# Performance work log

Hardware: AMD Instinct MI355X
Metric: run time of the kernel (lower is better)

## Reference

```python
import jax, jax.numpy as jnp
import numpy as np

# Binarize: forward sign(x) in {-1,+1} (sign(0) -> +1), backward straight-through
# estimator (identity gradient), matching the standard ebnn Binarize autograd fn.
@jax.custom_vjp
def binarize(x):
    return jnp.where(x >= 0, 1.0, -1.0).astype(x.dtype)

def _bin_fwd(x):
    return binarize(x), None

def _bin_bwd(_, g):
    return (g,)  # straight-through

binarize.defvjp(_bin_fwd, _bin_bwd)


def setup_inputs() -> dict:
    key = jax.random.key(0)
    kx, kw = jax.random.split(key)
    N, Cin, H, W = 32, 256, 56, 56
    Cout, K = 256, 3
    x = jax.random.normal(kx, (N, Cin, H, W), dtype=jnp.float32)
    # xavier_normal init for conv weight
    fan_in = Cin * K * K
    fan_out = Cout * K * K
    std = float(np.sqrt(2.0 / (fan_in + fan_out)))
    w = jax.random.normal(kw, (Cout, Cin, K, K), dtype=jnp.float32) * std
    b = jnp.zeros((Cout,), dtype=jnp.float32)
    return {"x": x, "w": w, "b": b}


def reference(x, w, b):
    # binarize input (binarize_input=True) and weights, then standard conv2d
    xb = binarize(x)
    wb = binarize(w)
    out = jax.lax.conv_general_dilated(
        xb, wb,
        window_strides=(1, 1),
        padding=((1, 1), (1, 1)),
        rhs_dilation=(1, 1),
        dimension_numbers=("NCHW", "OIHW", "NCHW"),
        feature_group_count=1,
    )
    return out + b[None, :, None, None]
```

## Files before the change

kernel.cpp:

```cpp
#include <hip/hip_runtime.h>
#include <stdint.h>


#define NBATCH 32
#define CIN    256
#define COUT   256
#define HH     56
#define WW     56
#define HW     (HH*WW)
#define NPIX   (NBATCH*HW)

#define PW    58
#define PROW  (PW*8)
#define PIMG  (PW*PW*8)

#define XP_BYTES  ((size_t)NBATCH * PIMG * 4)
#define WQ_BYTES  ((size_t)9 * 8 * 256 * 32)

typedef int i32x4  __attribute__((ext_vector_type(4)));
typedef int i32x16 __attribute__((ext_vector_type(16)));

__global__ __launch_bounds__(256) void pack_x_kernel(
    const float* __restrict__ x, uint32_t* __restrict__ xp)
{
    int lane = threadIdx.x & 63;
    int wv   = threadIdx.x >> 6;
    int pix  = blockIdx.x * 64 + lane;
    int n  = pix / HW;
    int hw = pix - n * HW;
    int h  = hw / WW;
    int w_ = hw - h * WW;
    const float* xb = x + ((size_t)n * CIN + (size_t)wv * 64) * HW + hw;

    uint32_t w0 = 0, w1 = 0;
    #pragma unroll
    for (int j = 0; j < 32; ++j) {
        w0 |= (xb[(size_t)j * HW]        >= 0.0f ? 1u : 0u) << j;
        w1 |= (xb[(size_t)(j + 32) * HW] >= 0.0f ? 1u : 0u) << j;
    }
    uint32_t* dst = xp + (size_t)n * PIMG + (size_t)(h + 1) * PROW
                       + (size_t)(w_ + 1) * 8 + wv * 2;
    *(uint2*)dst = make_uint2(w0, w1);
}

__global__ __launch_bounds__(256) void pack_w2_kernel(
    const float* __restrict__ w, int8_t* __restrict__ wq)
{
    int co = blockIdx.x, ci = threadIdx.x;
    const float* wb = w + ((size_t)co * CIN + ci) * 9;
    int c8 = ci >> 5, s = ci & 31;
    #pragma unroll
    for (int t = 0; t < 9; ++t) {
        wq[((size_t)(t * 8 + c8) * 256 + co) * 32 + s] =
            (wb[t] >= 0.0f) ? (int8_t)1 : (int8_t)-1;
    }
}

__global__ __launch_bounds__(512, 4) void bconv_kernel(
    const uint32_t* __restrict__ xp, const int8_t* __restrict__ wq,
    const float* __restrict__ bias, float* __restrict__ out)
{
    __shared__ __align__(16) int8_t xt[4][66][256];
    __shared__ float bsh[256];

    int bx = blockIdx.x;
    int n  = bx / 28;
    int hb = bx - n * 28;
    int h  = hb * 2;
    int tid = threadIdx.x, lane = tid & 63, wv = tid >> 6;

    if (tid < 256) bsh[tid] = bias[tid];

    const uint32_t* xpb = xp + (size_t)n * PIMG;
    for (int e = tid; e < 4 * 66 * 64; e += 512) {
        int pr  = e / (66 * 64);
        int rem = e - pr * (66 * 64);
        int col = rem >> 6;
        int d   = rem & 63;
        int prg = h + pr;
        bool val = (prg >= 1) & (prg <= 56) & (col >= 1) & (col <= 56);
        uint32_t wvv = 0;
        if (val) wvv = xpb[(size_t)prg * PROW + col * 8 + (d >> 3)];
        uint32_t nib = (wvv >> ((d & 7) * 4)) & 0xFu;
        uint32_t sp  = (nib * 0x00204081u) & 0x01010101u;
        uint32_t o   = val ? __builtin_amdgcn_perm(0u, 0x000001FFu, sp) : 0u;
        uint32_t ba  = (uint32_t)((((pr * 66 + col) << 8) | (d << 2))
                                  ^ ((col & 15) << 4));
        *(uint32_t*)((char*)&xt[0][0][0] + ba) = o;
    }
    __syncthreads();

    int l31  = lane & 31;
    int hi16 = (lane >> 5) << 4;
    const int8_t* wql = wq + ((size_t)(wv * 32 + l31)) * 32 + hi16;
    const char* xtb = (const char*)&xt[0][0][0];

    for (int cb = 0; cb < 2; ++cb) {
        i32x16 accA = {0}, accB = {0};

        for (int dw = 0; dw < 3; ++dw) {
            int col = l31 + cb * 32 + dw;
            int sw  = (col & 15) << 4;
            const char* xc = xtb + (col << 8);
            const int8_t* wa0 = wql + (size_t)(dw * 8) * 8192;
            #pragma unroll
            for (int c8 = 0; c8 < 8; ++c8) {
                int sx = ((c8 << 5) + hi16) ^ sw;
                i32x4 b0 = *(const i32x4*)(xc + ((0 * 66) << 8) + sx);
                i32x4 b1 = *(const i32x4*)(xc + ((1 * 66) << 8) + sx);
                i32x4 b2 = *(const i32x4*)(xc + ((2 * 66) << 8) + sx);
                i32x4 b3 = *(const i32x4*)(xc + ((3 * 66) << 8) + sx);
                const int8_t* wa = wa0 + (size_t)c8 * 8192;
                i32x4 a0v = *(const i32x4*)(wa);
                i32x4 a1v = *(const i32x4*)(wa + 196608);
                i32x4 a2v = *(const i32x4*)(wa + 393216);
                accA = __builtin_amdgcn_mfma_i32_32x32x32_i8(a0v, b0, accA, 0, 0, 0);
                accB = __builtin_amdgcn_mfma_i32_32x32x32_i8(a0v, b1, accB, 0, 0, 0);
                accA = __builtin_amdgcn_mfma_i32_32x32x32_i8(a1v, b1, accA, 0, 0, 0);
                accB = __builtin_amdgcn_mfma_i32_32x32x32_i8(a1v, b2, accB, 0, 0, 0);
                accA = __builtin_amdgcn_mfma_i32_32x32x32_i8(a2v, b2, accA, 0, 0, 0);
                accB = __builtin_amdgcn_mfma_i32_32x32x32_i8(a2v, b3, accB, 0, 0, 0);
            }
        }

        int pix = cb * 32 + l31;
        if (pix < WW) {
            float* op = out + (size_t)n * COUT * HW + (size_t)h * WW + pix;
            #pragma unroll
            for (int r = 0; r < 16; ++r) {
                int row = (r & 3) + 8 * (r >> 2) + ((lane >> 5) << 2);
                int co  = (wv << 5) + row;
                float bb = bsh[co];
                op[(size_t)co * HW]      = (float)accA[r] + bb;
                op[(size_t)co * HW + WW] = (float)accB[r] + bb;
            }
        }
    }
}

extern "C" void kernel_launch(void* const* d_in, const int* in_sizes, int n_in,
                              void* d_out, int out_size, void* d_ws, size_t ws_size,
                              hipStream_t stream) {
    const float* x = (const float*)d_in[0];
    const float* w = (const float*)d_in[1];
    const float* b = (const float*)d_in[2];
    float* out = (float*)d_out;

    uint32_t* xp = (uint32_t*)d_ws;
    int8_t*   wq = (int8_t*)((char*)d_ws + XP_BYTES);

    pack_x_kernel<<<NPIX / 64, 256, 0, stream>>>(x, xp);
    pack_w2_kernel<<<COUT, 256, 0, stream>>>(w, wq);

    bconv_kernel<<<NBATCH * (HH / 2), 512, 0, stream>>>(xp, wq, b, out);
}
```

Baseline: 97.17 us.

## Relayout packed weights per wave and software-pipeline operand loads across MFMA groups

Weights are repacked so that each 32-output-channel group holds its three dh taps for each (dw, c8) step contiguously, 1 KB apart. The inner loop is flattened into 24 fully unrolled steps, and the global weight and LDS activation loads for the next step are issued before the current step's six MFMAs. The goal is to hide load latency behind MFMA work and improve locality of the weight fetches. The cost is more live registers for the double-buffered operands, which could affect occupancy under launch_bounds(512,4).

```diff
diff --git a/kernel.cpp b/kernel.cpp
--- a/kernel.cpp
+++ b/kernel.cpp
@@ -15,7 +15,7 @@
 #define PIMG  (PW*PW*8)
 
 #define XP_BYTES  ((size_t)NBATCH * PIMG * 4)
-#define WQ_BYTES  ((size_t)9 * 8 * 256 * 32)
+#define WQ_BYTES  ((size_t)8 * 72 * 1024)
 
 typedef int i32x4  __attribute__((ext_vector_type(4)));
 typedef int i32x16 __attribute__((ext_vector_type(16)));
@@ -43,21 +43,41 @@
     *(uint2*)dst = make_uint2(w0, w1);
 }
 
-__global__ __launch_bounds__(256) void pack_w2_kernel(
-    const float* __restrict__ w, int8_t* __restrict__ wq)
+__global__ __launch_bounds__(256) void pack_w3_kernel(
+    const float* __restrict__ w, int8_t* __restrict__ wq3)
 {
     int co = blockIdx.x, ci = threadIdx.x;
     const float* wb = w + ((size_t)co * CIN + ci) * 9;
-    int c8 = ci >> 5, s = ci & 31;
+    int cog = co >> 5, l = co & 31, c8 = ci >> 5, s = ci & 31;
+    int8_t* base = wq3 + (size_t)cog * 73728 + (size_t)l * 32 + s;
     #pragma unroll
-    for (int t = 0; t < 9; ++t) {
-        wq[((size_t)(t * 8 + c8) * 256 + co) * 32 + s] =
-            (wb[t] >= 0.0f) ? (int8_t)1 : (int8_t)-1;
+    for (int dh = 0; dh < 3; ++dh) {
+        #pragma unroll
+        for (int dw = 0; dw < 3; ++dw) {
+            int t = dh * 3 + dw;
+            base[(size_t)((dw * 8 + c8) * 3 + dh) * 1024] =
+                (wb[t] >= 0.0f) ? (int8_t)1 : (int8_t)-1;
+        }
     }
 }
 
+#define LOADG(gi, A0, A1, A2, B0, B1, B2, B3) { \
+    const int dw_ = (gi) >> 3, c8_ = (gi) & 7; \
+    const int col_ = l31 + cb * 32 + dw_; \
+    const int sw_ = (col_ & 15) << 4; \
+    const char* xc_ = xtb + (col_ << 8); \
+    const int sx_ = ((c8_ << 5) + hi16) ^ sw_; \
+    B0 = *(const i32x4*)(xc_ + ((0 * 66) << 8) + sx_); \
+    B1 = *(const i32x4*)(xc_ + ((1 * 66) << 8) + sx_); \
+    B2 = *(const i32x4*)(xc_ + ((2 * 66) << 8) + sx_); \
+    B3 = *(const i32x4*)(xc_ + ((3 * 66) << 8) + sx_); \
+    const char* wa_ = wqc + (size_t)((dw_ * 8 + c8_) * 3) * 1024; \
+    A0 = *(const i32x4*)(wa_); \
+    A1 = *(const i32x4*)(wa_ + 1024); \
+    A2 = *(const i32x4*)(wa_ + 2048); }
+
 __global__ __launch_bounds__(512, 4) void bconv_kernel(
-    const uint32_t* __restrict__ xp, const int8_t* __restrict__ wq,
+    const uint32_t* __restrict__ xp, const int8_t* __restrict__ wq3,
     const float* __restrict__ bias, float* __restrict__ out)
 {
     __shared__ __align__(16) int8_t xt[4][66][256];
@@ -92,34 +112,28 @@
 
     int l31  = lane & 31;
     int hi16 = (lane >> 5) << 4;
-    const int8_t* wql = wq + ((size_t)(wv * 32 + l31)) * 32 + hi16;
+    const char* wqc = (const char*)wq3 + (size_t)wv * 73728
+                    + (size_t)l31 * 32 + hi16;
     const char* xtb = (const char*)&xt[0][0][0];
 
     for (int cb = 0; cb < 2; ++cb) {
         i32x16 accA = {0}, accB = {0};
+        i32x4 a0, a1, a2, b0, b1, b2, b3;
+        i32x4 na0, na1, na2, nb0, nb1, nb2, nb3;
 
-        for (int dw = 0; dw < 3; ++dw) {
-            int col = l31 + cb * 32 + dw;
-            int sw  = (col & 15) << 4;
-            const char* xc = xtb + (col << 8);
-            const int8_t* wa0 = wql + (size_t)(dw * 8) * 8192;
-            #pragma unroll
-            for (int c8 = 0; c8 < 8; ++c8) {
-                int sx = ((c8 << 5) + hi16) ^ sw;
-                i32x4 b0 = *(const i32x4*)(xc + ((0 * 66) << 8) + sx);
-                i32x4 b1 = *(const i32x4*)(xc + ((1 * 66) << 8) + sx);
-                i32x4 b2 = *(const i32x4*)(xc + ((2 * 66) << 8) + sx);
-                i32x4 b3 = *(const i32x4*)(xc + ((3 * 66) << 8) + sx);
-                const int8_t* wa = wa0 + (size_t)c8 * 8192;
-                i32x4 a0v = *(const i32x4*)(wa);
-                i32x4 a1v = *(const i32x4*)(wa + 196608);
-                i32x4 a2v = *(const i32x4*)(wa + 393216);
-                accA = __builtin_amdgcn_mfma_i32_32x32x32_i8(a0v, b0, accA, 0, 0, 0);
-                accB = __builtin_amdgcn_mfma_i32_32x32x32_i8(a0v, b1, accB, 0, 0, 0);
-                accA = __builtin_amdgcn_mfma_i32_32x32x32_i8(a1v, b1, accA, 0, 0, 0);
-                accB = __builtin_amdgcn_mfma_i32_32x32x32_i8(a1v, b2, accB, 0, 0, 0);
-                accA = __builtin_amdgcn_mfma_i32_32x32x32_i8(a2v, b2, accA, 0, 0, 0);
-                accB = __builtin_amdgcn_mfma_i32_32x32x32_i8(a2v, b3, accB, 0, 0, 0);
+        LOADG(0, a0, a1, a2, b0, b1, b2, b3)
+        #pragma unroll
+        for (int gi = 0; gi < 24; ++gi) {
+            if (gi < 23) { LOADG(gi + 1, na0, na1, na2, nb0, nb1, nb2, nb3) }
+            accA = __builtin_amdgcn_mfma_i32_32x32x32_i8(a0, b0, accA, 0, 0, 0);
+            accB = __builtin_amdgcn_mfma_i32_32x32x32_i8(a0, b1, accB, 0, 0, 0);
+            accA = __builtin_amdgcn_mfma_i32_32x32x32_i8(a1, b1, accA, 0, 0, 0);
+            accB = __builtin_amdgcn_mfma_i32_32x32x32_i8(a1, b2, accB, 0, 0, 0);
+            accA = __builtin_amdgcn_mfma_i32_32x32x32_i8(a2, b2, accA, 0, 0, 0);
+            accB = __builtin_amdgcn_mfma_i32_32x32x32_i8(a2, b3, accB, 0, 0, 0);
+            if (gi < 23) {
+                a0 = na0; a1 = na1; a2 = na2;
+                b0 = nb0; b1 = nb1; b2 = nb2; b3 = nb3;
             }
         }
 
@@ -146,11 +160,11 @@
     const float* b = (const float*)d_in[2];
     float* out = (float*)d_out;
 
-    uint32_t* xp = (uint32_t*)d_ws;
-    int8_t*   wq = (int8_t*)((char*)d_ws + XP_BYTES);
+    uint32_t* xp  = (uint32_t*)d_ws;
+    int8_t*   wq3 = (int8_t*)((char*)d_ws + XP_BYTES);
 
     pack_x_kernel<<<NPIX / 64, 256, 0, stream>>>(x, xp);
-    pack_w2_kernel<<<COUT, 256, 0, stream>>>(w, wq);
+    pack_w3_kernel<<<COUT, 256, 0, stream>>>(w, wq3);
 
-    bconv_kernel<<<NBATCH * (HH / 2), 512, 0, stream>>>(xp, wq, b, out);
+    bconv_kernel<<<NBATCH * (HH / 2), 512, 0, stream>>>(xp, wq3, b, out);
 }
```

Result: slower. 123.5 us (+27.1%).

## Prefetch all weight fragments per tap and double-buffer LDS operand loads

Applied to the files above, without the earlier changes.

For each horizontal tap, all 24 weight fragments are loaded from global memory into registers up front. The shared-memory input fragments are then double-buffered so the next channel group's LDS reads are issued while the current group's MFMAs run. The launch-bounds occupancy hint drops from 4 to 2 blocks per CU to leave room for the extra registers, and the cb/dw loops are kept rolled. The intent is to hide global and LDS latency behind MFMA work, at the cost of higher register pressure and fewer resident waves.

```diff
diff --git a/kernel.cpp b/kernel.cpp
--- a/kernel.cpp
+++ b/kernel.cpp
@@ -56,7 +56,22 @@
     }
 }
 
-__global__ __launch_bounds__(512, 4) void bconv_kernel(
+#define LOADB(c8x, B0, B1, B2, B3) { \
+    const int sx_ = (((c8x) << 5) + hi16) ^ sw; \
+    B0 = *(const i32x4*)(xc + ((0 * 66) << 8) + sx_); \
+    B1 = *(const i32x4*)(xc + ((1 * 66) << 8) + sx_); \
+    B2 = *(const i32x4*)(xc + ((2 * 66) << 8) + sx_); \
+    B3 = *(const i32x4*)(xc + ((3 * 66) << 8) + sx_); }
+
+#define MFMA6(A0, A1, A2, B0, B1, B2, B3) \
+    accA = __builtin_amdgcn_mfma_i32_32x32x32_i8(A0, B0, accA, 0, 0, 0); \
+    accB = __builtin_amdgcn_mfma_i32_32x32x32_i8(A0, B1, accB, 0, 0, 0); \
+    accA = __builtin_amdgcn_mfma_i32_32x32x32_i8(A1, B1, accA, 0, 0, 0); \
+    accB = __builtin_amdgcn_mfma_i32_32x32x32_i8(A1, B2, accB, 0, 0, 0); \
+    accA = __builtin_amdgcn_mfma_i32_32x32x32_i8(A2, B2, accA, 0, 0, 0); \
+    accB = __builtin_amdgcn_mfma_i32_32x32x32_i8(A2, B3, accB, 0, 0, 0);
+
+__global__ __launch_bounds__(512, 2) void bconv_kernel(
     const uint32_t* __restrict__ xp, const int8_t* __restrict__ wq,
     const float* __restrict__ bias, float* __restrict__ out)
 {
@@ -92,34 +107,36 @@
 
     int l31  = lane & 31;
     int hi16 = (lane >> 5) << 4;
-    const int8_t* wql = wq + ((size_t)(wv * 32 + l31)) * 32 + hi16;
+    const char* wql = (const char*)wq + (size_t)(wv * 32 + l31) * 32 + hi16;
     const char* xtb = (const char*)&xt[0][0][0];
 
+    #pragma unroll 1
     for (int cb = 0; cb < 2; ++cb) {
         i32x16 accA = {0}, accB = {0};
 
+        #pragma unroll 1
         for (int dw = 0; dw < 3; ++dw) {
             int col = l31 + cb * 32 + dw;
             int sw  = (col & 15) << 4;
             const char* xc = xtb + (col << 8);
-            const int8_t* wa0 = wql + (size_t)(dw * 8) * 8192;
+
+            i32x4 aa[8][3];
             #pragma unroll
             for (int c8 = 0; c8 < 8; ++c8) {
-                int sx = ((c8 << 5) + hi16) ^ sw;
-                i32x4 b0 = *(const i32x4*)(xc + ((0 * 66) << 8) + sx);
-                i32x4 b1 = *(const i32x4*)(xc + ((1 * 66) << 8) + sx);
-                i32x4 b2 = *(const i32x4*)(xc + ((2 * 66) << 8) + sx);
-                i32x4 b3 = *(const i32x4*)(xc + ((3 * 66) << 8) + sx);
-                const int8_t* wa = wa0 + (size_t)c8 * 8192;
-                i32x4 a0v = *(const i32x4*)(wa);
-                i32x4 a1v = *(const i32x4*)(wa + 196608);
-                i32x4 a2v = *(const i32x4*)(wa + 393216);
-                accA = __builtin_amdgcn_mfma_i32_32x32x32_i8(a0v, b0, accA, 0, 0, 0);
-                accB = __builtin_amdgcn_mfma_i32_32x32x32_i8(a0v, b1, accB, 0, 0, 0);
-                accA = __builtin_amdgcn_mfma_i32_32x32x32_i8(a1v, b1, accA, 0, 0, 0);
-                accB = __builtin_amdgcn_mfma_i32_32x32x32_i8(a1v, b2, accB, 0, 0, 0);
-                accA = __builtin_amdgcn_mfma_i32_32x32x32_i8(a2v, b2, accA, 0, 0, 0);
-                accB = __builtin_amdgcn_mfma_i32_32x32x32_i8(a2v, b3, accB, 0, 0, 0);
+                const char* wa = wql + (size_t)((dw * 8 + c8)) * 8192;
+                aa[c8][0] = *(const i32x4*)(wa);
+                aa[c8][1] = *(const i32x4*)(wa + 196608);
+                aa[c8][2] = *(const i32x4*)(wa + 393216);
+            }
+
+            i32x4 b0, b1, b2, b3, d0, d1, d2, d3;
+            LOADB(0, b0, b1, b2, b3)
+            #pragma unroll
+            for (int gp = 0; gp < 4; ++gp) {
+                LOADB(2 * gp + 1, d0, d1, d2, d3)
+                MFMA6(aa[2 * gp][0], aa[2 * gp][1], aa[2 * gp][2], b0, b1, b2, b3)
+                if (gp < 3) { LOADB(2 * gp + 2, b0, b1, b2, b3) }
+                MFMA6(aa[2 * gp + 1][0], aa[2 * gp + 1][1], aa[2 * gp + 1][2], d0, d1, d2, d3)
             }
         }
 
```

New measurement: 108.7 us. 11.9% more time.

## Split column halves across separate blocks and shrink LDS tile

Applied to the files above, without the earlier changes.

Each block now handles only one 32-column half of a two-row output strip instead of looping over both halves, which doubles the grid size. The LDS input tile shrinks from 66 to 34 columns and launch bounds are raised to 6 blocks per CU, aiming for higher occupancy and better latency hiding. The cost is redundant staging of the overlapping halo columns and twice as many weight fetches from global/L2 per output.

```diff
diff --git a/kernel.cpp b/kernel.cpp
--- a/kernel.cpp
+++ b/kernel.cpp
@@ -56,35 +56,41 @@
     }
 }
 
-__global__ __launch_bounds__(512, 4) void bconv_kernel(
+#define MFMA(ACC, A, B) \
+    ACC = __builtin_amdgcn_mfma_i32_32x32x32_i8(A, B, ACC, 0, 0, 0);
+
+__global__ __launch_bounds__(512, 6) void bconv_kernel(
     const uint32_t* __restrict__ xp, const int8_t* __restrict__ wq,
     const float* __restrict__ bias, float* __restrict__ out)
 {
-    __shared__ __align__(16) int8_t xt[4][66][256];
+    __shared__ __align__(16) int8_t xt[4][34][256];
     __shared__ float bsh[256];
 
-    int bx = blockIdx.x;
-    int n  = bx / 28;
-    int hb = bx - n * 28;
-    int h  = hb * 2;
+    int bx  = blockIdx.x;
+    int cb2 = bx & 1;
+    int t2  = bx >> 1;
+    int n   = t2 / 28;
+    int hb  = t2 - n * 28;
+    int h   = hb * 2;
     int tid = threadIdx.x, lane = tid & 63, wv = tid >> 6;
 
     if (tid < 256) bsh[tid] = bias[tid];
 
     const uint32_t* xpb = xp + (size_t)n * PIMG;
-    for (int e = tid; e < 4 * 66 * 64; e += 512) {
-        int pr  = e / (66 * 64);
-        int rem = e - pr * (66 * 64);
+    for (int e = tid; e < 4 * 34 * 64; e += 512) {
+        int pr  = e / (34 * 64);
+        int rem = e - pr * (34 * 64);
         int col = rem >> 6;
         int d   = rem & 63;
         int prg = h + pr;
-        bool val = (prg >= 1) & (prg <= 56) & (col >= 1) & (col <= 56);
+        int gcol = cb2 * 32 + col;
+        bool val = (prg >= 1) & (prg <= 56) & (gcol >= 1) & (gcol <= 56);
         uint32_t wvv = 0;
-        if (val) wvv = xpb[(size_t)prg * PROW + col * 8 + (d >> 3)];
+        if (val) wvv = xpb[(size_t)prg * PROW + gcol * 8 + (d >> 3)];
         uint32_t nib = (wvv >> ((d & 7) * 4)) & 0xFu;
         uint32_t sp  = (nib * 0x00204081u) & 0x01010101u;
         uint32_t o   = val ? __builtin_amdgcn_perm(0u, 0x000001FFu, sp) : 0u;
-        uint32_t ba  = (uint32_t)((((pr * 66 + col) << 8) | (d << 2))
+        uint32_t ba  = (uint32_t)((((pr * 34 + col) << 8) | (d << 2))
                                   ^ ((col & 15) << 4));
         *(uint32_t*)((char*)&xt[0][0][0] + ba) = o;
     }
@@ -92,48 +98,43 @@
 
     int l31  = lane & 31;
     int hi16 = (lane >> 5) << 4;
-    const int8_t* wql = wq + ((size_t)(wv * 32 + l31)) * 32 + hi16;
+    const char* wql = (const char*)wq + (size_t)(wv * 32 + l31) * 32 + hi16;
     const char* xtb = (const char*)&xt[0][0][0];
 
-    for (int cb = 0; cb < 2; ++cb) {
-        i32x16 accA = {0}, accB = {0};
+    i32x16 accA = {0}, accB = {0};
 
-        for (int dw = 0; dw < 3; ++dw) {
-            int col = l31 + cb * 32 + dw;
-            int sw  = (col & 15) << 4;
-            const char* xc = xtb + (col << 8);
-            const int8_t* wa0 = wql + (size_t)(dw * 8) * 8192;
-            #pragma unroll
-            for (int c8 = 0; c8 < 8; ++c8) {
-                int sx = ((c8 << 5) + hi16) ^ sw;
-                i32x4 b0 = *(const i32x4*)(xc + ((0 * 66) << 8) + sx);
-                i32x4 b1 = *(const i32x4*)(xc + ((1 * 66) << 8) + sx);
-                i32x4 b2 = *(const i32x4*)(xc + ((2 * 66) << 8) + sx);
-                i32x4 b3 = *(const i32x4*)(xc + ((3 * 66) << 8) + sx);
-                const int8_t* wa = wa0 + (size_t)c8 * 8192;
-                i32x4 a0v = *(const i32x4*)(wa);
-                i32x4 a1v = *(const i32x4*)(wa + 196608);
-                i32x4 a2v = *(const i32x4*)(wa + 393216);
-                accA = __builtin_amdgcn_mfma_i32_32x32x32_i8(a0v, b0, accA, 0, 0, 0);
-                accB = __builtin_amdgcn_mfma_i32_32x32x32_i8(a0v, b1, accB, 0, 0, 0);
-                accA = __builtin_amdgcn_mfma_i32_32x32x32_i8(a1v, b1, accA, 0, 0, 0);
-                accB = __builtin_amdgcn_mfma_i32_32x32x32_i8(a1v, b2, accB, 0, 0, 0);
-                accA = __builtin_amdgcn_mfma_i32_32x32x32_i8(a2v, b2, accA, 0, 0, 0);
-                accB = __builtin_amdgcn_mfma_i32_32x32x32_i8(a2v, b3, accB, 0, 0, 0);
-            }
+    #pragma unroll 1
+    for (int dw = 0; dw < 3; ++dw) {
+        int col0 = l31 + dw;
+        int sw   = (col0 & 15) << 4;
+        const char* xc = xtb + (col0 << 8);
+        #pragma unroll
+        for (int c8 = 0; c8 < 8; ++c8) {
+            int sx = ((c8 << 5) + hi16) ^ sw;
+            i32x4 b0 = *(const i32x4*)(xc + ((0 * 34) << 8) + sx);
+            i32x4 b1 = *(const i32x4*)(xc + ((1 * 34) << 8) + sx);
+            i32x4 b2 = *(const i32x4*)(xc + ((2 * 34) << 8) + sx);
+            i32x4 b3 = *(const i32x4*)(xc + ((3 * 34) << 8) + sx);
+            const char* wa = wql + (size_t)(dw * 8 + c8) * 8192;
+            i32x4 a0 = *(const i32x4*)(wa);
+            i32x4 a1 = *(const i32x4*)(wa + 196608);
+            i32x4 a2 = *(const i32x4*)(wa + 393216);
+            MFMA(accA, a0, b0) MFMA(accB, a0, b1)
+            MFMA(accA, a1, b1) MFMA(accB, a1, b2)
+            MFMA(accA, a2, b2) MFMA(accB, a2, b3)
         }
+    }
 
-        int pix = cb * 32 + l31;
-        if (pix < WW) {
-            float* op = out + (size_t)n * COUT * HW + (size_t)h * WW + pix;
-            #pragma unroll
-            for (int r = 0; r < 16; ++r) {
-                int row = (r & 3) + 8 * (r >> 2) + ((lane >> 5) << 2);
-                int co  = (wv << 5) + row;
-                float bb = bsh[co];
-                op[(size_t)co * HW]      = (float)accA[r] + bb;
-                op[(size_t)co * HW + WW] = (float)accB[r] + bb;
-            }
+    int pix = cb2 * 32 + l31;
+    if (pix < WW) {
+        float* op = out + (size_t)n * COUT * HW + (size_t)h * WW + pix;
+        #pragma unroll
+        for (int r = 0; r < 16; ++r) {
+            int row = (r & 3) + 8 * (r >> 2) + ((lane >> 5) << 2);
+            int co  = (wv << 5) + row;
+            float bb = bsh[co];
+            op[(size_t)co * HW]      = (float)accA[r] + bb;
+            op[(size_t)co * HW + WW] = (float)accB[r] + bb;
         }
     }
 }
@@ -152,5 +153,5 @@
     pack_x_kernel<<<NPIX / 64, 256, 0, stream>>>(x, xp);
     pack_w2_kernel<<<COUT, 256, 0, stream>>>(w, wq);
 
-    bconv_kernel<<<NBATCH * (HH / 2), 512, 0, stream>>>(xp, wq, b, out);
+    bconv_kernel<<<NBATCH * 28 * 2, 512, 0, stream>>>(xp, wq, b, out);
 }
```

New measurement: 100.0 us. +3.0%, slower.
